# Kernel tuning notes

Hardware: AMD Instinct MI355X
Metric: run time of the kernel (lower is better)

The kernel has to match this reference:

```python
import jax, jax.numpy as jnp
import numpy as np

B, S, E, H = 2, 2048, 1024, 16
D = E // H  # head_dim = 64


def setup_inputs() -> dict:
    key = jax.random.key(0)
    ks = jax.random.split(key, 5)
    return {
        "hidden_states": jax.random.normal(ks[0], (B, S, E), jnp.float32),
        "c_attn_w": jax.random.normal(ks[1], (E, 3 * E), jnp.float32) * 0.02,
        "c_attn_b": jax.random.normal(ks[2], (3 * E,), jnp.float32) * 0.02,
        "c_proj_w": jax.random.normal(ks[3], (E, E), jnp.float32) * 0.02,
        "c_proj_b": jax.random.normal(ks[4], (E,), jnp.float32) * 0.02,
    }


def reference(hidden_states, c_attn_w, c_attn_b, c_proj_w, c_proj_b):
    # Conv1D: y = x @ W + b, W is [in, out]
    qkv = hidden_states @ c_attn_w + c_attn_b            # [B,S,3E]
    q, k, v = jnp.split(qkv, 3, axis=-1)                 # each [B,S,E]

    def split_heads(t):
        return t.reshape(B, S, H, D).transpose(0, 2, 1, 3)  # [B,H,S,D]

    q, k, v = split_heads(q), split_heads(k), split_heads(v)

    # scores scaled by 1/sqrt(head_dim) (scale_attn_weights=True)
    scores = jnp.einsum("bhqd,bhkd->bhqk", q, k) / jnp.asarray(
        np.sqrt(D), dtype=q.dtype
    )
    # causal mask: torch.where(causal, scores, finfo.min)
    causal = jnp.tril(jnp.ones((S, S), dtype=bool))
    mask_value = jnp.finfo(scores.dtype).min
    scores = jnp.where(causal[None, None], scores, mask_value)

    attn = jax.nn.softmax(scores, axis=-1)               # [B,H,S,S]
    out = jnp.einsum("bhqk,bhkd->bhqd", attn, v)          # [B,H,S,D]
    out = out.transpose(0, 2, 1, 3).reshape(B, S, E)      # merge heads
    out = out @ c_proj_w + c_proj_b                       # c_proj
    return out
```

## Files before the change

### kernel.cpp

```cpp
#include <hip/hip_runtime.h>
#include <stdint.h>

#define LOG2E 1.4426950408889634f
#define QSCALE (0.125f * LOG2E)

using u16 = unsigned short;
using u32 = unsigned int;

typedef __attribute__((ext_vector_type(8))) short short8;
typedef __attribute__((ext_vector_type(4))) float f32x4;
typedef __attribute__((ext_vector_type(16))) float f32x16;

__device__ __forceinline__ u16 f32_bf16(float f) {
  union { float f; u32 u; } v; v.f = f;
  u32 u = v.u;
  u += 0x7FFF + ((u >> 16) & 1);
  return (u16)(u >> 16);
}

__device__ __forceinline__ float max3f(float a, float b, float c) {
  return fmaxf(fmaxf(a, b), c);
}

__device__ __forceinline__ void gload_lds16(const void* g, void* l) {
  __builtin_amdgcn_global_load_lds(
      (const __attribute__((address_space(1))) u32*)(uintptr_t)g,
      (__attribute__((address_space(3))) u32*)(u32)(uintptr_t)l, 16, 0, 0);
}


__global__ __launch_bounds__(256) void cvt_f32_bf16(const float* __restrict__ in,
                                                    u16* __restrict__ out, int n4) {
  for (int i = blockIdx.x * blockDim.x + threadIdx.x; i < n4;
       i += gridDim.x * blockDim.x) {
    float4 v = ((const float4*)in)[i];
    union { u16 h[4]; uint2 u; } o;
    o.h[0] = f32_bf16(v.x); o.h[1] = f32_bf16(v.y);
    o.h[2] = f32_bf16(v.z); o.h[3] = f32_bf16(v.w);
    ((uint2*)out)[i] = o.u;
  }
}

__global__ __launch_bounds__(256) void transpose_bf16(const float* __restrict__ in,
                                                      u16* __restrict__ out,
                                                      int K, int N) {
  __shared__ float t[32][33];
  const int n0 = blockIdx.x * 32, k0 = blockIdx.y * 32;
  const int tx = threadIdx.x, ty = threadIdx.y;
#pragma unroll
  for (int j = 0; j < 32; j += 8)
    t[ty + j][tx] = in[(size_t)(k0 + ty + j) * N + n0 + tx];
  __syncthreads();
#pragma unroll
  for (int j = 0; j < 32; j += 8)
    out[(size_t)(n0 + ty + j) * K + k0 + tx] = f32_bf16(t[tx][ty + j]);
}

template <int MODE>
__global__ __launch_bounds__(256) void gemm_bt3(
    const u16* __restrict__ A, const u16* __restrict__ Bt,
    const float* __restrict__ bias,
    u16* __restrict__ qb, u16* __restrict__ kb, u16* __restrict__ vtb,
    float* __restrict__ fout) {
  __shared__ u16 lA[4096];
  __shared__ u16 lB[4096];
  const int tid = threadIdx.x;
  const int w = tid >> 6, l = tid & 63;
  const int l15 = l & 15, l4 = l >> 4;
  const int wr = w >> 1, wc = w & 1;
  const int bm = blockIdx.y, bn = blockIdx.x;
  const size_t m0 = (size_t)bm * 128, n0 = (size_t)bn * 128;

  f32x4 acc[4][4] = {};

  const int c = w * 64 + l;
  const int pair0 = c >> 3, s80 = c & 7;
  const int us8 = s80 ^ (pair0 & 7);
  const int grow = 2 * pair0 + (us8 >> 2);
  const int kslot = us8 & 3;
  const u16* gA = A + (m0 + grow) * 1024 + kslot * 8;
  const u16* gB = Bt + (n0 + grow) * 1024 + kslot * 8;
  u16* lAw = lA + w * 512;
  u16* lBw = lB + w * 512;

  for (int k0 = 0; k0 < 1024; k0 += 32) {
    gload_lds16(gA + k0, lAw);
    gload_lds16(gA + k0 + 64 * 1024, lAw + 2048);
    gload_lds16(gB + k0, lBw);
    gload_lds16(gB + k0 + 64 * 1024, lBw + 2048);
    __syncthreads();
    short8 af[4], bf[4];
#pragma unroll
    for (int mI = 0; mI < 4; ++mI) {
      const int row = wr * 64 + mI * 16 + l15;
      const int pr = row >> 1;
      const int s8 = (((row & 1) << 2) | l4) ^ (pr & 7);
      af[mI] = *(const short8*)((const char*)lA + pr * 128 + s8 * 16);
    }
#pragma unroll
    for (int n = 0; n < 4; ++n) {
      const int row = wc * 64 + n * 16 + l15;
      const int pr = row >> 1;
      const int s8 = (((row & 1) << 2) | l4) ^ (pr & 7);
      bf[n] = *(const short8*)((const char*)lB + pr * 128 + s8 * 16);
    }
#pragma unroll
    for (int mI = 0; mI < 4; ++mI)
#pragma unroll
      for (int n = 0; n < 4; ++n)
        acc[mI][n] = __builtin_amdgcn_mfma_f32_16x16x32_bf16(af[mI], bf[n], acc[mI][n], 0, 0, 0);
    __syncthreads();
  }

  if (MODE == 0) {
#pragma unroll
    for (int mI = 0; mI < 4; ++mI) {
      const int row = (int)m0 + wr * 64 + mI * 16 + (l4 << 2);
      const int b = row >> 11, s = row & 2047;
#pragma unroll
      for (int n = 0; n < 4; ++n) {
        const int col = (int)n0 + wc * 64 + n * 16 + l15;
        const int part = col >> 10;
        const int h = (col & 1023) >> 6, d = col & 63;
        const float bv = bias[col];
        const size_t bh = (size_t)(b * 16 + h);
#pragma unroll
        for (int r = 0; r < 4; ++r) {
          const float v = acc[mI][n][r] + bv;
          const int ss = s + r;
          if (part == 0)
            qb[(bh * 2048 + ss) * 64 + d] = f32_bf16(v * QSCALE);
          else if (part == 1)
            kb[(bh * 2048 + ss) * 64 + d] = f32_bf16(v);
          else
            vtb[(bh * 64 + d) * 2048 + ss] = f32_bf16(v);
        }
      }
    }
  } else {
#pragma unroll
    for (int mI = 0; mI < 4; ++mI) {
      const size_t row = m0 + wr * 64 + mI * 16 + (l4 << 2);
#pragma unroll
      for (int n = 0; n < 4; ++n) {
        const size_t col = n0 + wc * 64 + n * 16 + l15;
        const float bv = bias[col];
#pragma unroll
        for (int r = 0; r < 4; ++r)
          fout[(row + r) * 1024 + col] = acc[mI][n][r] + bv;
      }
    }
  }
}

__global__ __launch_bounds__(128) void attn_fwd7(const u16* __restrict__ Qb,
                                                 const u16* __restrict__ Kb,
                                                 const u16* __restrict__ Vt,
                                                 u16* __restrict__ AO) {
  __shared__ u16 lK[2][4096];
  __shared__ u16 lV[2][4096];
  const int tid = threadIdx.x;
  const int l = tid & 63, w = tid >> 6;
  const int lq = l & 31, hi = l >> 5;
  const int bid = blockIdx.x;
  const int xcd = bid & 7, idx = bid >> 3;
  const int bh = xcd * 4 + (idx & 3);
  const int qb = 31 - (idx >> 2);
  const int q = qb * 64 + w * 32 + lq;
  const int NT = qb + 1;

  const u16* Qh = Qb + (size_t)bh * 131072;
  const u16* Kh = Kb + (size_t)bh * 131072;
  const u16* Vh = Vt + (size_t)bh * 131072;

  short8 qf[4];
#pragma unroll
  for (int kk = 0; kk < 4; ++kk)
    qf[kk] = *(const short8*)&Qh[(size_t)q * 64 + kk * 16 + hi * 8];

  f32x16 oA = {}, oB = {};
  float m = -3.0e38f, lsum = 0.f;

  const int srow = l >> 3, sslot = l & 7;
  const int swz = ((sslot ^ srow) << 3);
  const u16* kbase = Kh + (32 * w + srow) * 64 + swz;
  const u16* vbase = Vh + (size_t)(32 * w + srow) * 2048 + swz;

  auto stage = [&](int buf, int c) {
    const u16* ks = kbase + c * 4096;
    const u16* vs = vbase + c * 64;
    char* kd = (char*)&lK[buf][0] + w * 4096;
    char* vd = (char*)&lV[buf][0] + w * 4096;
#pragma unroll
    for (int i = 0; i < 4; ++i) {
      gload_lds16(ks + 512 * i, kd + 1024 * i);
      gload_lds16(vs + 16384 * i, vd + 1024 * i);
    }
  };

  const int swsl = (lq & 7);

  auto pack16 = [&](const f32x16& st, short8& lo, short8& hi8) {
    u32 pk[8];
#pragma unroll
    for (int t2 = 0; t2 < 8; ++t2)
      asm("v_cvt_pk_bf16_f32 %0, %1, %2" : "=v"(pk[t2]) : "v"(st[2 * t2]), "v"(st[2 * t2 + 1]));
    u32 a0 = pk[0], a1 = pk[2]; asm("v_permlane32_swap_b32 %0, %1" : "+v"(a0), "+v"(a1));
    u32 a2 = pk[1], a3 = pk[3]; asm("v_permlane32_swap_b32 %0, %1" : "+v"(a2), "+v"(a3));
    u32 c0 = pk[4], c1 = pk[6]; asm("v_permlane32_swap_b32 %0, %1" : "+v"(c0), "+v"(c1));
    u32 c2 = pk[5], c3 = pk[7]; asm("v_permlane32_swap_b32 %0, %1" : "+v"(c2), "+v"(c3));
    union { u32 u[4]; short8 s; } f0, f1;
    f0.u[0] = a0; f0.u[1] = a2; f0.u[2] = a1; f0.u[3] = a3;
    f1.u[0] = c0; f1.u[1] = c2; f1.u[2] = c1; f1.u[3] = c3;
    lo = f0.s; hi8 = f1.s;
  };

  auto body64 = [&](int buf, bool mask2) {
    const char* kb = (const char*)&lK[buf][0] + lq * 128;
    const char* vb = (const char*)&lV[buf][0] + lq * 128;
    short8 kf0[4], kf1[4];
#pragma unroll
    for (int kk = 0; kk < 4; ++kk) {
      const int sl = ((2 * kk + hi) ^ swsl) << 4;
      kf0[kk] = *(const short8*)(kb + sl);
      kf1[kk] = *(const short8*)(kb + 4096 + sl);
    }
    f32x16 st0 = {}, st1 = {};
    __builtin_amdgcn_s_setprio(1);
#pragma unroll
    for (int kk = 0; kk < 4; ++kk)
      st0 = __builtin_amdgcn_mfma_f32_32x32x16_bf16(kf0[kk], qf[kk], st0, 0, 0, 0);
#pragma unroll
    for (int kk = 0; kk < 4; ++kk)
      st1 = __builtin_amdgcn_mfma_f32_32x32x16_bf16(kf1[kk], qf[kk], st1, 0, 0, 0);
    __builtin_amdgcn_s_setprio(0);

    short8 vfA[4], vfB[4];
#pragma unroll
    for (int ks = 0; ks < 4; ++ks) {
      const int sl = ((2 * ks + hi) ^ swsl) << 4;
      vfA[ks] = *(const short8*)(vb + sl);
      vfB[ks] = *(const short8*)(vb + 4096 + sl);
    }

    if (mask2) {
      const int qm = lq - hi * 4;
#pragma unroll
      for (int r = 0; r < 16; ++r) {
        const int t = (r & 3) + 8 * (r >> 2);
        if (t > qm) st1[r] = -3.0e38f;
      }
    }

    float a0 = max3f(st0[0], st0[1], st0[2]);
    float a1 = max3f(st0[3], st0[4], st0[5]);
    float a2 = max3f(st0[6], st0[7], st0[8]);
    float a3 = max3f(st0[9], st0[10], st0[11]);
    float a4 = max3f(st0[12], st0[13], st0[14]);
    float a5 = max3f(st0[15], st1[0], st1[1]);
    float a6 = max3f(st1[2], st1[3], st1[4]);
    float a7 = max3f(st1[5], st1[6], st1[7]);
    float a8 = max3f(st1[8], st1[9], st1[10]);
    float a9 = max3f(st1[11], st1[12], st1[13]);
    float a10 = fmaxf(st1[14], st1[15]);
    float b0 = max3f(a0, a1, a2);
    float b1 = max3f(a3, a4, a5);
    float b2 = max3f(a6, a7, a8);
    float b3 = max3f(a9, a10, b0);
    float pm = max3f(b1, b2, b3);
    pm = fmaxf(pm, __shfl_xor(pm, 32));

    if (!__all(pm <= m + 8.0f)) {
      const float mn = fmaxf(m, pm);
      const float alpha = __builtin_amdgcn_exp2f(m - mn);
      lsum *= alpha;
#pragma unroll
      for (int r = 0; r < 16; ++r) { oA[r] *= alpha; oB[r] *= alpha; }
      m = mn;
    }

#pragma unroll
    for (int r = 0; r < 16; ++r) st0[r] = __builtin_amdgcn_exp2f(st0[r] - m);
#pragma unroll
    for (int r = 0; r < 16; ++r) st1[r] = __builtin_amdgcn_exp2f(st1[r] - m);

    float s0 = (st0[0] + st0[1]) + (st0[2] + st0[3]);
    float s1 = (st0[4] + st0[5]) + (st0[6] + st0[7]);
    float s2 = (st0[8] + st0[9]) + (st0[10] + st0[11]);
    float s3 = (st0[12] + st0[13]) + (st0[14] + st0[15]);
    float s4 = (st1[0] + st1[1]) + (st1[2] + st1[3]);
    float s5 = (st1[4] + st1[5]) + (st1[6] + st1[7]);
    float s6 = (st1[8] + st1[9]) + (st1[10] + st1[11]);
    float s7 = (st1[12] + st1[13]) + (st1[14] + st1[15]);
    float rs = ((s0 + s1) + (s2 + s3)) + ((s4 + s5) + (s6 + s7));
    rs += __shfl_xor(rs, 32);
    lsum += rs;

    short8 pf0, pf1, pf2, pf3;
    pack16(st0, pf0, pf1);
    pack16(st1, pf2, pf3);

    __builtin_amdgcn_s_setprio(1);
    oA = __builtin_amdgcn_mfma_f32_32x32x16_bf16(vfA[0], pf0, oA, 0, 0, 0);
    oA = __builtin_amdgcn_mfma_f32_32x32x16_bf16(vfA[1], pf1, oA, 0, 0, 0);
    oA = __builtin_amdgcn_mfma_f32_32x32x16_bf16(vfA[2], pf2, oA, 0, 0, 0);
    oA = __builtin_amdgcn_mfma_f32_32x32x16_bf16(vfA[3], pf3, oA, 0, 0, 0);
    oB = __builtin_amdgcn_mfma_f32_32x32x16_bf16(vfB[0], pf0, oB, 0, 0, 0);
    oB = __builtin_amdgcn_mfma_f32_32x32x16_bf16(vfB[1], pf1, oB, 0, 0, 0);
    oB = __builtin_amdgcn_mfma_f32_32x32x16_bf16(vfB[2], pf2, oB, 0, 0, 0);
    oB = __builtin_amdgcn_mfma_f32_32x32x16_bf16(vfB[3], pf3, oB, 0, 0, 0);
    __builtin_amdgcn_s_setprio(0);
  };

  auto body32m = [&](int buf) {
    const char* kb = (const char*)&lK[buf][0] + lq * 128;
    const char* vb = (const char*)&lV[buf][0] + lq * 128;
    short8 kf0[4];
#pragma unroll
    for (int kk = 0; kk < 4; ++kk)
      kf0[kk] = *(const short8*)(kb + (((2 * kk + hi) ^ swsl) << 4));
    f32x16 st0 = {};
    __builtin_amdgcn_s_setprio(1);
#pragma unroll
    for (int kk = 0; kk < 4; ++kk)
      st0 = __builtin_amdgcn_mfma_f32_32x32x16_bf16(kf0[kk], qf[kk], st0, 0, 0, 0);
    __builtin_amdgcn_s_setprio(0);

    short8 vfA[2], vfB[2];
#pragma unroll
    for (int ks = 0; ks < 2; ++ks) {
      const int sl = ((2 * ks + hi) ^ swsl) << 4;
      vfA[ks] = *(const short8*)(vb + sl);
      vfB[ks] = *(const short8*)(vb + 4096 + sl);
    }

    const int qm = lq - hi * 4;
#pragma unroll
    for (int r = 0; r < 16; ++r) {
      const int t = (r & 3) + 8 * (r >> 2);
      if (t > qm) st0[r] = -3.0e38f;
    }
    float a0 = max3f(st0[0], st0[1], st0[2]);
    float a1 = max3f(st0[3], st0[4], st0[5]);
    float a2 = max3f(st0[6], st0[7], st0[8]);
    float a3 = max3f(st0[9], st0[10], st0[11]);
    float a4 = max3f(st0[12], st0[13], st0[14]);
    float b0 = max3f(a0, a1, a2);
    float b1 = max3f(a3, a4, st0[15]);
    float pm = fmaxf(b0, b1);
    pm = fmaxf(pm, __shfl_xor(pm, 32));
    if (!__all(pm <= m + 8.0f)) {
      const float mn = fmaxf(m, pm);
      const float alpha = __builtin_amdgcn_exp2f(m - mn);
      lsum *= alpha;
#pragma unroll
      for (int r = 0; r < 16; ++r) { oA[r] *= alpha; oB[r] *= alpha; }
      m = mn;
    }
#pragma unroll
    for (int r = 0; r < 16; ++r) st0[r] = __builtin_amdgcn_exp2f(st0[r] - m);
    float s0 = (st0[0] + st0[1]) + (st0[2] + st0[3]);
    float s1 = (st0[4] + st0[5]) + (st0[6] + st0[7]);
    float s2 = (st0[8] + st0[9]) + (st0[10] + st0[11]);
    float s3 = (st0[12] + st0[13]) + (st0[14] + st0[15]);
    float rs = (s0 + s1) + (s2 + s3);
    rs += __shfl_xor(rs, 32);
    lsum += rs;

    short8 pf0, pf1;
    pack16(st0, pf0, pf1);
    __builtin_amdgcn_s_setprio(1);
    oA = __builtin_amdgcn_mfma_f32_32x32x16_bf16(vfA[0], pf0, oA, 0, 0, 0);
    oA = __builtin_amdgcn_mfma_f32_32x32x16_bf16(vfA[1], pf1, oA, 0, 0, 0);
    oB = __builtin_amdgcn_mfma_f32_32x32x16_bf16(vfB[0], pf0, oB, 0, 0, 0);
    oB = __builtin_amdgcn_mfma_f32_32x32x16_bf16(vfB[1], pf1, oB, 0, 0, 0);
    __builtin_amdgcn_s_setprio(0);
  };

  stage(0, 0);
  __syncthreads();
  int cur = 0;
  for (int c = 0; c < NT; ++c) {
    if (c + 1 < NT) stage(cur ^ 1, c + 1);
    if (c < qb) body64(cur, false);
    else { if (w) body64(cur, true); else body32m(cur); }
    __syncthreads();
    cur ^= 1;
  }

  const float rl = __builtin_amdgcn_rcpf(lsum);
  const int b = bh >> 4, h = bh & 15;
  u16* orow = AO + ((size_t)(b * 2048 + q)) * 1024 + h * 64;
#pragma unroll
  for (int g = 0; g < 4; ++g) {
    float e0 = oA[4 * g] * rl, e1 = oA[4 * g + 1] * rl;
    float e2 = oA[4 * g + 2] * rl, e3 = oA[4 * g + 3] * rl;
    float f0 = oB[4 * g] * rl, f1 = oB[4 * g + 1] * rl;
    float f2 = oB[4 * g + 2] * rl, f3 = oB[4 * g + 3] * rl;
    u32 w0, w1, w2, w3;
    asm("v_cvt_pk_bf16_f32 %0, %1, %2" : "=v"(w0) : "v"(e0), "v"(e1));
    asm("v_cvt_pk_bf16_f32 %0, %1, %2" : "=v"(w1) : "v"(e2), "v"(e3));
    asm("v_cvt_pk_bf16_f32 %0, %1, %2" : "=v"(w2) : "v"(f0), "v"(f1));
    asm("v_cvt_pk_bf16_f32 %0, %1, %2" : "=v"(w3) : "v"(f2), "v"(f3));
    uint2 uA; uA.x = w0; uA.y = w1;
    uint2 uB; uB.x = w2; uB.y = w3;
    *(uint2*)&orow[8 * g + 4 * hi] = uA;
    *(uint2*)&orow[32 + 8 * g + 4 * hi] = uB;
  }
}


extern "C" void kernel_launch(void* const* d_in, const int* in_sizes, int n_in,
                              void* d_out, int out_size, void* d_ws, size_t ws_size,
                              hipStream_t stream) {
  const float* hs = (const float*)d_in[0];
  const float* w1 = (const float*)d_in[1];
  const float* b1 = (const float*)d_in[2];
  const float* w2 = (const float*)d_in[3];
  const float* b2 = (const float*)d_in[4];
  float* out = (float*)d_out;

  char* ws = (char*)d_ws;
  u16* Xb  = (u16*)(ws);
  u16* W1t = (u16*)(ws + (8ull  << 20));
  u16* W2t = (u16*)(ws + (14ull << 20));
  u16* Qb  = (u16*)(ws + (16ull << 20));
  u16* Kb  = (u16*)(ws + (24ull << 20));
  u16* Vtb = (u16*)(ws + (32ull << 20));
  u16* AO  = (u16*)(ws + (40ull << 20));

  cvt_f32_bf16<<<dim3(2048), dim3(256), 0, stream>>>(hs, Xb, 4096 * 1024 / 4);
  transpose_bf16<<<dim3(96, 32), dim3(32, 8), 0, stream>>>(w1, W1t, 1024, 3072);
  transpose_bf16<<<dim3(32, 32), dim3(32, 8), 0, stream>>>(w2, W2t, 1024, 1024);
  gemm_bt3<0><<<dim3(24, 32), dim3(256), 0, stream>>>(Xb, W1t, b1, Qb, Kb, Vtb, nullptr);
  attn_fwd7<<<dim3(1024), dim3(128), 0, stream>>>(Qb, Kb, Vtb, AO);
  gemm_bt3<1><<<dim3(8, 32), dim3(256), 0, stream>>>(AO, W2t, b2, nullptr, nullptr, nullptr, out);
}
```

Baseline: 126.6 us.

## Double-buffer GEMM LDS staging and use 4-wave 128-row attention blocks

```diff
diff --git a/kernel.cpp b/kernel.cpp
--- a/kernel.cpp
+++ b/kernel.cpp
@@ -57,13 +57,13 @@
 }
 
 template <int MODE>
-__global__ __launch_bounds__(256) void gemm_bt3(
+__global__ __launch_bounds__(256) void gemm_db(
     const u16* __restrict__ A, const u16* __restrict__ Bt,
     const float* __restrict__ bias,
     u16* __restrict__ qb, u16* __restrict__ kb, u16* __restrict__ vtb,
     float* __restrict__ fout) {
-  __shared__ u16 lA[4096];
-  __shared__ u16 lB[4096];
+  __shared__ u16 lA[2][4096];
+  __shared__ u16 lB[2][4096];
   const int tid = threadIdx.x;
   const int w = tid >> 6, l = tid & 63;
   const int l15 = l & 15, l4 = l >> 4;
@@ -80,36 +80,48 @@
   const int kslot = us8 & 3;
   const u16* gA = A + (m0 + grow) * 1024 + kslot * 8;
   const u16* gB = Bt + (n0 + grow) * 1024 + kslot * 8;
-  u16* lAw = lA + w * 512;
-  u16* lBw = lB + w * 512;
-
-  for (int k0 = 0; k0 < 1024; k0 += 32) {
-    gload_lds16(gA + k0, lAw);
-    gload_lds16(gA + k0 + 64 * 1024, lAw + 2048);
-    gload_lds16(gB + k0, lBw);
-    gload_lds16(gB + k0 + 64 * 1024, lBw + 2048);
-    __syncthreads();
+
+  auto stage = [&](int buf, int t) {
+    const int k0 = t * 32;
+    gload_lds16(gA + k0, lA[buf] + w * 512);
+    gload_lds16(gA + k0 + 64 * 1024, lA[buf] + 2048 + w * 512);
+    gload_lds16(gB + k0, lB[buf] + w * 512);
+    gload_lds16(gB + k0 + 64 * 1024, lB[buf] + 2048 + w * 512);
+  };
+
+  stage(0, 0);
+  stage(1, 1);
+
+  for (int t = 0; t < 32; ++t) {
+    const int buf = t & 1;
+    if (t == 31) asm volatile("s_waitcnt vmcnt(0)" ::: "memory");
+    else         asm volatile("s_waitcnt vmcnt(4)" ::: "memory");
+    __builtin_amdgcn_s_barrier();
+    __builtin_amdgcn_sched_barrier(0);
     short8 af[4], bf[4];
 #pragma unroll
     for (int mI = 0; mI < 4; ++mI) {
       const int row = wr * 64 + mI * 16 + l15;
       const int pr = row >> 1;
       const int s8 = (((row & 1) << 2) | l4) ^ (pr & 7);
-      af[mI] = *(const short8*)((const char*)lA + pr * 128 + s8 * 16);
+      af[mI] = *(const short8*)((const char*)lA[buf] + pr * 128 + s8 * 16);
     }
 #pragma unroll
     for (int n = 0; n < 4; ++n) {
       const int row = wc * 64 + n * 16 + l15;
       const int pr = row >> 1;
       const int s8 = (((row & 1) << 2) | l4) ^ (pr & 7);
-      bf[n] = *(const short8*)((const char*)lB + pr * 128 + s8 * 16);
-    }
+      bf[n] = *(const short8*)((const char*)lB[buf] + pr * 128 + s8 * 16);
+    }
+    __builtin_amdgcn_s_setprio(1);
 #pragma unroll
     for (int mI = 0; mI < 4; ++mI)
 #pragma unroll
       for (int n = 0; n < 4; ++n)
         acc[mI][n] = __builtin_amdgcn_mfma_f32_16x16x32_bf16(af[mI], bf[n], acc[mI][n], 0, 0, 0);
-    __syncthreads();
+    __builtin_amdgcn_s_setprio(0);
+    __builtin_amdgcn_s_barrier();
+    if (t + 2 < 32) stage(buf, t + 2);
   }
 
   if (MODE == 0) {
@@ -153,7 +165,7 @@
   }
 }
 
-__global__ __launch_bounds__(128) void attn_fwd7(const u16* __restrict__ Qb,
+__global__ __launch_bounds__(256) void attn_fwd6(const u16* __restrict__ Qb,
                                                  const u16* __restrict__ Kb,
                                                  const u16* __restrict__ Vt,
                                                  u16* __restrict__ AO) {
@@ -165,9 +177,11 @@
   const int bid = blockIdx.x;
   const int xcd = bid & 7, idx = bid >> 3;
   const int bh = xcd * 4 + (idx & 3);
-  const int qb = 31 - (idx >> 2);
-  const int q = qb * 64 + w * 32 + lq;
-  const int NT = qb + 1;
+  const int qb = 15 - (idx >> 2);
+  const int qw = qb * 128 + w * 32;
+  const int q = qw + lq;
+  const int cdiag = 2 * qb + (w >> 1);
+  const int NT = 2 * qb + 2;
 
   const u16* Qh = Qb + (size_t)bh * 131072;
   const u16* Kh = Kb + (size_t)bh * 131072;
@@ -183,19 +197,20 @@
 
   const int srow = l >> 3, sslot = l & 7;
   const int swz = ((sslot ^ srow) << 3);
-  const u16* kbase = Kh + (32 * w + srow) * 64 + swz;
-  const u16* vbase = Vh + (size_t)(32 * w + srow) * 2048 + swz;
+  const u16* kbase = Kh + (16 * w + srow) * 64 + swz;
+  const u16* vbase = Vh + (size_t)(16 * w + srow) * 2048 + swz;
+  char* lKw0 = (char*)&lK[0][0] + 2 * w * 1024;
+  char* lVw0 = (char*)&lV[0][0] + 2 * w * 1024;
 
   auto stage = [&](int buf, int c) {
     const u16* ks = kbase + c * 4096;
     const u16* vs = vbase + c * 64;
-    char* kd = (char*)&lK[buf][0] + w * 4096;
-    char* vd = (char*)&lV[buf][0] + w * 4096;
-#pragma unroll
-    for (int i = 0; i < 4; ++i) {
-      gload_lds16(ks + 512 * i, kd + 1024 * i);
-      gload_lds16(vs + 16384 * i, vd + 1024 * i);
-    }
+    char* kd = lKw0 + buf * 8192;
+    char* vd = lVw0 + buf * 8192;
+    gload_lds16(ks, kd);
+    gload_lds16(ks + 512, kd + 1024);
+    gload_lds16(vs, vd);
+    gload_lds16(vs + 16384, vd + 1024);
   };
 
   const int swsl = (lq & 7);
@@ -382,8 +397,8 @@
   int cur = 0;
   for (int c = 0; c < NT; ++c) {
     if (c + 1 < NT) stage(cur ^ 1, c + 1);
-    if (c < qb) body64(cur, false);
-    else { if (w) body64(cur, true); else body32m(cur); }
+    if (c < cdiag) body64(cur, false);
+    else if (c == cdiag) { if (w & 1) body64(cur, true); else body32m(cur); }
     __syncthreads();
     cur ^= 1;
   }
@@ -432,7 +447,7 @@
   cvt_f32_bf16<<<dim3(2048), dim3(256), 0, stream>>>(hs, Xb, 4096 * 1024 / 4);
   transpose_bf16<<<dim3(96, 32), dim3(32, 8), 0, stream>>>(w1, W1t, 1024, 3072);
   transpose_bf16<<<dim3(32, 32), dim3(32, 8), 0, stream>>>(w2, W2t, 1024, 1024);
-  gemm_bt3<0><<<dim3(24, 32), dim3(256), 0, stream>>>(Xb, W1t, b1, Qb, Kb, Vtb, nullptr);
-  attn_fwd7<<<dim3(1024), dim3(128), 0, stream>>>(Qb, Kb, Vtb, AO);
-  gemm_bt3<1><<<dim3(8, 32), dim3(256), 0, stream>>>(AO, W2t, b2, nullptr, nullptr, nullptr, out);
-}
+  gemm_db<0><<<dim3(24, 32), dim3(256), 0, stream>>>(Xb, W1t, b1, Qb, Kb, Vtb, nullptr);
+  attn_fwd6<<<dim3(512), dim3(256), 0, stream>>>(Qb, Kb, Vtb, AO);
+  gemm_db<1><<<dim3(8, 32), dim3(256), 0, stream>>>(AO, W2t, b2, nullptr, nullptr, nullptr, out);
+}
```

Result: faster. 117.4 us (-7.2%).
